# Kernel optimization log

Measured on AMD Instinct MI355X. Metric: run time of the kernel, lower is better.

Reference implementation:

```python
import jax, jax.numpy as jnp
import numpy as np

N = 100000      # nodes
E = 1600000     # edges
F_IN = 128      # num_feat
H = 128         # hidden_dim
EMB = 64        # node_embedding_dim
HL = 256        # hidden_dim_linear


def setup_inputs() -> dict:
    key = jax.random.key(0)
    ks = jax.random.split(key, 12)
    def w(k, fan_in, shape):
        return jax.random.normal(k, shape, dtype=jnp.float32) / np.sqrt(fan_in)
    x = jax.random.normal(ks[0], (N, F_IN), dtype=jnp.float32)
    edge_index = jax.random.randint(ks[1], (2, E), 0, N, dtype=jnp.int32)
    return {
        "x": x,
        "edge_index": edge_index,
        "W0": w(ks[2], F_IN, (F_IN, H)), "b0": jnp.zeros((H,), jnp.float32),
        "W1": w(ks[3], H, (H, H)),       "b1": jnp.zeros((H,), jnp.float32),
        "W2": w(ks[4], H, (H, EMB)),     "b2": jnp.zeros((EMB,), jnp.float32),
        "lw1": w(ks[5], 2 * EMB, (2 * EMB, HL)), "lb1": jnp.zeros((HL,), jnp.float32),
        "lw2": w(ks[6], HL, (HL, 1)),            "lb2": jnp.zeros((1,), jnp.float32),
    }


def _gcn_forward(x, edge_index, W0, b0, W1, b1, W2, b2, lw1, lb1, lw2, lb2):
    src, dst = edge_index[0], edge_index[1]
    # add self loops (PyG GCNConv default) -- shared across layers
    loop = jnp.arange(N, dtype=src.dtype)
    s = jnp.concatenate([src, loop])
    d = jnp.concatenate([dst, loop])
    # symmetric normalization: deg counts incoming edges incl. self loop (>=1)
    deg = jax.ops.segment_sum(jnp.ones_like(d, dtype=x.dtype), d, num_segments=N)
    norm = jax.lax.rsqrt(deg[s] * deg[d])  # [E+N]

    def conv(h, W, b):
        hw = h @ W                                   # small GEMM [N, out]
        msg = hw[s] * norm[:, None]                  # gather + scale [E+N, out]
        agg = jax.ops.segment_sum(msg, d, num_segments=N)
        return agg + b

    z = jax.nn.relu(conv(x, W0, b0))
    z = jax.nn.relu(conv(z, W1, b1))
    z = jax.nn.relu(conv(z, W2, b2))                 # [N, EMB]  (dropout: eval mode, no-op)

    # edge classifier: gather both endpoints, cat, MLP, sigmoid
    h = jnp.concatenate([z[src], z[dst]], axis=1)    # [E, 2*EMB]
    h = jax.nn.relu(h @ lw1 + lb1)
    return jax.nn.sigmoid(h @ lw2 + lb2)             # [E, 1]


def reference(x, edge_index, W0, b0, W1, b1, W2, b2, lw1, lb1, lw2, lb2):
    return _gcn_forward(x, edge_index, W0, b0, W1, b1, W2, b2, lw1, lb1, lw2, lb2)
```

## Files before the change

### kernel.cpp

```cpp
#include <hip/hip_runtime.h>

#define NNODES 100000
#define NEDGES 1600000
#define NBLK 391
#define NSLICE 8
#define SLICEW 12500

typedef __attribute__((ext_vector_type(8))) short bf16x8;
typedef __attribute__((ext_vector_type(4))) float f32x4;

__device__ __forceinline__ unsigned short f2bf(float f) {
  unsigned int u = __float_as_uint(f);
  u = (u + 0x7FFFu + ((u >> 16) & 1u)) >> 16;
  return (unsigned short)u;
}
__device__ __forceinline__ float bf2f(unsigned short h) {
  return __uint_as_float(((unsigned int)h) << 16);
}

__global__ void count_kernel(const int* __restrict__ dst, int* __restrict__ cntD) {
  int slice = blockIdx.x & (NSLICE - 1);
  int e = (blockIdx.x >> 3) * 256 + threadIdx.x;
  if (e >= NEDGES) return;
  int d = dst[e];
  int lo = slice * SLICEW;
  if (d >= lo && d < lo + SLICEW) atomicAdd(&cntD[d], 1);
}

__global__ void scanA_kernel(const int* __restrict__ cntD, int* __restrict__ blockSum) {
  __shared__ int sh[256];
  int v = blockIdx.x * 256 + threadIdx.x;
  sh[threadIdx.x] = (v < NNODES) ? cntD[v] : 0;
  __syncthreads();
  for (int off = 128; off; off >>= 1) {
    if (threadIdx.x < off) sh[threadIdx.x] += sh[threadIdx.x + off];
    __syncthreads();
  }
  if (threadIdx.x == 0) blockSum[blockIdx.x] = sh[0];
}

__global__ void scanB_kernel(int* __restrict__ blockSum) {
  int lane = threadIdx.x;
  int carry = 0;
  for (int base = 0; base < NBLK; base += 64) {
    int i = base + lane;
    int c = (i < NBLK) ? blockSum[i] : 0;
    int pre = c;
#pragma unroll
    for (int off = 1; off < 64; off <<= 1) {
      int t = __shfl_up(pre, off);
      if (lane >= off) pre += t;
    }
    int tot = __shfl(pre, 63);
    if (i < NBLK) blockSum[i] = carry + pre - c;
    carry += tot;
  }
}

__global__ void scanC_kernel(const int* __restrict__ cntD, const int* __restrict__ blockSum,
                             int* __restrict__ startD, int* __restrict__ curD,
                             float* __restrict__ dis) {
  __shared__ int sh[256];
  int tid = threadIdx.x;
  int v = blockIdx.x * 256 + tid;
  int c = (v < NNODES) ? cntD[v] : 0;
  sh[tid] = c;
  __syncthreads();
  for (int off = 1; off < 256; off <<= 1) {
    int t = (tid >= off) ? sh[tid - off] : 0;
    __syncthreads();
    sh[tid] += t;
    __syncthreads();
  }
  if (v < NNODES) {
    int s = blockSum[blockIdx.x] + sh[tid] - c;
    startD[v] = s;
    curD[v] = s;
    dis[v] = rsqrtf((float)(c + 1));
  }
}

__global__ void fill_kernel(const int* __restrict__ src, const int* __restrict__ dst,
                            int* __restrict__ curD, int2* __restrict__ csrPair) {
  int slice = blockIdx.x & (NSLICE - 1);
  int e = (blockIdx.x >> 3) * 256 + threadIdx.x;
  if (e >= NEDGES) return;
  int d = dst[e];
  int lo = slice * SLICEW;
  if (d < lo || d >= lo + SLICEW) return;
  int s = src[e];
  int pd = atomicAdd(&curD[d], 1);
  csrPair[pd] = make_int2(s, e);
}

template <int K, int HOUT>
__global__ void pack_w_kernel(const float* __restrict__ W, unsigned short* __restrict__ Wp) {
  int idx = blockIdx.x * 256 + threadIdx.x;
  if (idx < K * HOUT) {
    int k = idx / HOUT, c = idx - k * HOUT;
    Wp[((size_t)((k >> 5) * HOUT + c)) * 32 + (k & 31)] = f2bf(W[idx]);
  }
}

__global__ void pack_lw1_kernel(const float* __restrict__ lw1, const float* __restrict__ lb1,
                                unsigned short* __restrict__ Wp, float* __restrict__ biasAB) {
  int idx = blockIdx.x * 256 + threadIdx.x;
  if (idx < 64 * 512) {
    int k = idx / 512, c = idx - k * 512;
    float v = (c < 256) ? lw1[k * 256 + c] : lw1[(64 + k) * 256 + (c - 256)];
    Wp[((size_t)((k >> 5) * 512 + c)) * 32 + (k & 31)] = f2bf(v);
  }
  if (idx < 512) biasAB[idx] = (idx < 256) ? lb1[idx] : 0.0f;
}

__global__ void cvt_x_kernel(const float* __restrict__ x, unsigned short* __restrict__ hi,
                             unsigned short* __restrict__ lo) {
  int idx = blockIdx.x * 256 + threadIdx.x;
  if (idx < NNODES * 32) {
    float4 v = ((const float4*)x)[idx];
    ushort4 h, l;
    h.x = f2bf(v.x); l.x = f2bf(v.x - bf2f(h.x));
    h.y = f2bf(v.y); l.y = f2bf(v.y - bf2f(h.y));
    h.z = f2bf(v.z); l.z = f2bf(v.z - bf2f(h.z));
    h.w = f2bf(v.w); l.w = f2bf(v.w - bf2f(h.w));
    ((ushort4*)hi)[idx] = h;
    ((ushort4*)lo)[idx] = l;
  }
}

template <int K, int HOUT, bool SCALE, bool BIAS>
__global__ __launch_bounds__(256)
void mgemm_kernel(const unsigned short* __restrict__ Xhi, const unsigned short* __restrict__ Xlo,
                  const unsigned short* __restrict__ Wp, const float* __restrict__ dis,
                  const float* __restrict__ bias, unsigned short* __restrict__ outb) {
  constexpr int KC = K / 32;
  const int tid = threadIdx.x;
  const int wave = tid >> 6;
  const int lane = tid & 63;
  const int lrow = lane & 15;
  const int lsub = lane >> 4;
  const int rowBase = blockIdx.x * 64 + wave * 16;
  int arow = rowBase + lrow;
  if (arow > NNODES - 1) arow = NNODES - 1;
  bf16x8 ahi[KC], alo[KC];
#pragma unroll
  for (int kc = 0; kc < KC; ++kc) {
    ahi[kc] = *(const bf16x8*)&Xhi[(size_t)arow * K + kc * 32 + lsub * 8];
    alo[kc] = *(const bf16x8*)&Xlo[(size_t)arow * K + kc * 32 + lsub * 8];
  }
  int orow[4];
  float dis4[4];
#pragma unroll
  for (int i = 0; i < 4; ++i) {
    orow[i] = rowBase + lsub * 4 + i;
    int rc = orow[i] < NNODES ? orow[i] : NNODES - 1;
    dis4[i] = SCALE ? dis[rc] : 1.0f;
  }
  for (int ct = 0; ct < HOUT / 16; ++ct) {
    int c = ct * 16 + lrow;
    f32x4 acc = {0.f, 0.f, 0.f, 0.f};
#pragma unroll
    for (int kc = 0; kc < KC; ++kc) {
      bf16x8 b = *(const bf16x8*)&Wp[((size_t)(kc * HOUT + c)) * 32 + lsub * 8];
      acc = __builtin_amdgcn_mfma_f32_16x16x32_bf16(ahi[kc], b, acc, 0, 0, 0);
      acc = __builtin_amdgcn_mfma_f32_16x16x32_bf16(alo[kc], b, acc, 0, 0, 0);
    }
    float bb = BIAS ? bias[c] : 0.0f;
#pragma unroll
    for (int i = 0; i < 4; ++i) {
      if (orow[i] < NNODES) {
        float v = acc[i];
        if (SCALE) v *= dis4[i];
        if (BIAS) v += bb;
        outb[(size_t)orow[i] * HOUT + c] = f2bf(v);
      }
    }
  }
}

template <int HOUT>
__global__ __launch_bounds__(256)
void agg_kernel(const unsigned short* __restrict__ hws, const int2* __restrict__ csrPair,
                const int* __restrict__ startA, const int* __restrict__ cnt,
                const float* __restrict__ dis, const float* __restrict__ bias,
                unsigned short* __restrict__ outHi, unsigned short* __restrict__ outLo) {
  int gid = blockIdx.x * 256 + threadIdx.x;
  int v = gid >> 6;
  int lane = gid & 63;
  constexpr int PER = HOUT / 64;
  float acc0 = 0.0f, acc1 = 0.0f;
  if constexpr (PER == 2) {
    unsigned int o = *(const unsigned int*)&hws[(size_t)v * HOUT + lane * 2];
    acc0 = __uint_as_float(o << 16);
    acc1 = __uint_as_float(o & 0xffff0000u);
  } else {
    acc0 = bf2f(hws[(size_t)v * HOUT + lane]);
  }
  int s0 = startA[v], c = cnt[v];
  for (int base = 0; base < c; base += 64) {
    int rem = c - base;
    int m = rem < 64 ? rem : 64;
    int idx = 0;
    if (lane < m) idx = csrPair[s0 + base + lane].x;
    int j = 0;
    for (; j + 4 <= m; j += 4) {
      int u0 = __shfl(idx, j);
      int u1 = __shfl(idx, j + 1);
      int u2 = __shfl(idx, j + 2);
      int u3 = __shfl(idx, j + 3);
      if constexpr (PER == 2) {
        unsigned int r0 = *(const unsigned int*)&hws[(size_t)u0 * HOUT + lane * 2];
        unsigned int r1 = *(const unsigned int*)&hws[(size_t)u1 * HOUT + lane * 2];
        unsigned int r2 = *(const unsigned int*)&hws[(size_t)u2 * HOUT + lane * 2];
        unsigned int r3 = *(const unsigned int*)&hws[(size_t)u3 * HOUT + lane * 2];
        acc0 += __uint_as_float(r0 << 16) + __uint_as_float(r1 << 16) +
                __uint_as_float(r2 << 16) + __uint_as_float(r3 << 16);
        acc1 += __uint_as_float(r0 & 0xffff0000u) + __uint_as_float(r1 & 0xffff0000u) +
                __uint_as_float(r2 & 0xffff0000u) + __uint_as_float(r3 & 0xffff0000u);
      } else {
        float r0 = bf2f(hws[(size_t)u0 * HOUT + lane]);
        float r1 = bf2f(hws[(size_t)u1 * HOUT + lane]);
        float r2 = bf2f(hws[(size_t)u2 * HOUT + lane]);
        float r3 = bf2f(hws[(size_t)u3 * HOUT + lane]);
        acc0 += (r0 + r1) + (r2 + r3);
      }
    }
    for (; j < m; ++j) {
      int u = __shfl(idx, j);
      if constexpr (PER == 2) {
        unsigned int r = *(const unsigned int*)&hws[(size_t)u * HOUT + lane * 2];
        acc0 += __uint_as_float(r << 16);
        acc1 += __uint_as_float(r & 0xffff0000u);
      } else {
        acc0 += bf2f(hws[(size_t)u * HOUT + lane]);
      }
    }
  }
  float d = dis[v];
  if constexpr (PER == 2) {
    float o0 = fmaf(d, acc0, bias[lane * 2]);
    float o1 = fmaf(d, acc1, bias[lane * 2 + 1]);
    o0 = o0 > 0.0f ? o0 : 0.0f;
    o1 = o1 > 0.0f ? o1 : 0.0f;
    ushort2 h, l;
    h.x = f2bf(o0); l.x = f2bf(o0 - bf2f(h.x));
    h.y = f2bf(o1); l.y = f2bf(o1 - bf2f(h.y));
    *(ushort2*)&outHi[(size_t)v * HOUT + lane * 2] = h;
    *(ushort2*)&outLo[(size_t)v * HOUT + lane * 2] = l;
  } else {
    float o0 = fmaf(d, acc0, bias[lane]);
    o0 = o0 > 0.0f ? o0 : 0.0f;
    unsigned short h = f2bf(o0);
    outHi[(size_t)v * HOUT + lane] = h;
    outLo[(size_t)v * HOUT + lane] = f2bf(o0 - bf2f(h));
  }
}

__global__ __launch_bounds__(256)
void edge_kernel(const unsigned short* __restrict__ AB,
                 const int2* __restrict__ csrPair,
                 const int* __restrict__ startD, const int* __restrict__ cntD,
                 const float* __restrict__ lw2,
                 float* __restrict__ out) {
  int gid = blockIdx.x * 256 + threadIdx.x;
  int v = gid >> 6;
  int lane = gid & 63;
  int sub = lane & 15;
  const unsigned int* Brow = (const unsigned int*)&AB[(size_t)v * 512 + 256 + sub * 16];
  uint4 br0 = *(const uint4*)Brow;
  uint4 br1 = *(const uint4*)(Brow + 4);
  float bq[16];
  {
    unsigned int u[8] = {br0.x, br0.y, br0.z, br0.w, br1.x, br1.y, br1.z, br1.w};
#pragma unroll
    for (int i = 0; i < 8; ++i) {
      bq[2 * i]     = __uint_as_float(u[i] << 16);
      bq[2 * i + 1] = __uint_as_float(u[i] & 0xffff0000u);
    }
  }
  float wv[16];
#pragma unroll
  for (int i = 0; i < 4; ++i) {
    float4 w4 = *(const float4*)&lw2[sub * 16 + i * 4];
    wv[4 * i] = w4.x; wv[4 * i + 1] = w4.y; wv[4 * i + 2] = w4.z; wv[4 * i + 3] = w4.w;
  }

  int s0 = startD[v], c = cntD[v];
  for (int base = 0; base < c; base += 64) {
    int rem = c - base;
    int m = rem < 64 ? rem : 64;
    int sj = 0, ej = 0;
    if (lane < m) {
      int2 p = csrPair[s0 + base + lane];
      sj = p.x; ej = p.y;
    }
    for (int j = 0; j < m; j += 4) {
      int ls = j + (lane >> 4);
      int lsc = ls < m ? ls : m - 1;
      int s = __shfl(sj, lsc);
      int e = __shfl(ej, lsc);
      const unsigned int* Arow = (const unsigned int*)&AB[(size_t)(unsigned)s * 512 + sub * 16];
      uint4 a0 = *(const uint4*)Arow;
      uint4 a1 = *(const uint4*)(Arow + 4);
      unsigned int au[8] = {a0.x, a0.y, a0.z, a0.w, a1.x, a1.y, a1.z, a1.w};
      float p0 = 0.f, p1 = 0.f, p2 = 0.f, p3 = 0.f;
#pragma unroll
      for (int i = 0; i < 4; ++i) {
        float hlo0 = __uint_as_float(au[2 * i] << 16) + bq[4 * i];
        float hhi0 = __uint_as_float(au[2 * i] & 0xffff0000u) + bq[4 * i + 1];
        float hlo1 = __uint_as_float(au[2 * i + 1] << 16) + bq[4 * i + 2];
        float hhi1 = __uint_as_float(au[2 * i + 1] & 0xffff0000u) + bq[4 * i + 3];
        hlo0 = hlo0 > 0.f ? hlo0 : 0.f;
        hhi0 = hhi0 > 0.f ? hhi0 : 0.f;
        hlo1 = hlo1 > 0.f ? hlo1 : 0.f;
        hhi1 = hhi1 > 0.f ? hhi1 : 0.f;
        p0 = fmaf(hlo0, wv[4 * i], p0);
        p1 = fmaf(hhi0, wv[4 * i + 1], p1);
        p2 = fmaf(hlo1, wv[4 * i + 2], p2);
        p3 = fmaf(hhi1, wv[4 * i + 3], p3);
      }
      float acc = (p0 + p1) + (p2 + p3);
      acc += __shfl_xor(acc, 1);
      acc += __shfl_xor(acc, 2);
      acc += __shfl_xor(acc, 4);
      acc += __shfl_xor(acc, 8);
      if (ls < m && sub == 0) out[e] = acc;
    }
  }
}

__global__ __launch_bounds__(256)
void sigmoid_kernel(float* __restrict__ out, const float* __restrict__ lb2) {
  int i = blockIdx.x * 256 + threadIdx.x;
  if (i < NEDGES) {
    float lb = lb2[0];
    out[i] = 1.0f / (1.0f + expf(-(out[i] + lb)));
  }
}

extern "C" void kernel_launch(void* const* d_in, const int* in_sizes, int n_in,
                              void* d_out, int out_size, void* d_ws, size_t ws_size,
                              hipStream_t stream) {
  const float* x   = (const float*)d_in[0];
  const int*   ei  = (const int*)d_in[1];
  const float* W0  = (const float*)d_in[2];
  const float* b0  = (const float*)d_in[3];
  const float* W1  = (const float*)d_in[4];
  const float* b1  = (const float*)d_in[5];
  const float* W2  = (const float*)d_in[6];
  const float* b2  = (const float*)d_in[7];
  const float* lw1 = (const float*)d_in[8];
  const float* lb1 = (const float*)d_in[9];
  const float* lw2 = (const float*)d_in[10];
  const float* lb2 = (const float*)d_in[11];
  float* out = (float*)d_out;
  const int* src = ei;
  const int* dst = ei + NEDGES;

  char* ws = (char*)d_ws;
  size_t off = 0;
  auto alloc = [&](size_t bytes) -> void* {
    void* p = ws + off;
    off += (bytes + 255) & ~(size_t)255;
    return p;
  };
  int*   cntD   = (int*)alloc((size_t)NNODES * 4);
  int*   startD = (int*)alloc((size_t)NNODES * 4);
  int*   curD   = (int*)alloc((size_t)NNODES * 4);
  float* dis    = (float*)alloc((size_t)NNODES * 4);
  int*   blockSum = (int*)alloc((size_t)NBLK * 4);
  int2*  csrPair= (int2*)alloc((size_t)NEDGES * 8);
  unsigned short* P16  = (unsigned short*)alloc((size_t)NNODES * 128 * 2);
  unsigned short* XQhi = (unsigned short*)alloc((size_t)NNODES * 128 * 2);
  unsigned short* XQlo = (unsigned short*)alloc((size_t)NNODES * 128 * 2);
  unsigned short* AB   = (unsigned short*)alloc((size_t)NNODES * 512 * 2);
  unsigned short* Wp0  = (unsigned short*)alloc((size_t)128 * 128 * 2);
  unsigned short* Wp1  = (unsigned short*)alloc((size_t)128 * 128 * 2);
  unsigned short* Wp2  = (unsigned short*)alloc((size_t)128 * 64 * 2);
  unsigned short* WpE  = (unsigned short*)alloc((size_t)64 * 512 * 2);
  float* biasAB = (float*)alloc(512 * 4);

  const int EB8 = NSLICE * ((NEDGES + 255) / 256);

  hipMemsetAsync(cntD, 0, (size_t)NNODES * 4, stream);
  count_kernel<<<EB8, 256, 0, stream>>>(dst, cntD);
  scanA_kernel<<<NBLK, 256, 0, stream>>>(cntD, blockSum);
  scanB_kernel<<<1, 64, 0, stream>>>(blockSum);
  scanC_kernel<<<NBLK, 256, 0, stream>>>(cntD, blockSum, startD, curD, dis);
  fill_kernel<<<EB8, 256, 0, stream>>>(src, dst, curD, csrPair);

  pack_w_kernel<128, 128><<<64, 256, 0, stream>>>(W0, Wp0);
  pack_w_kernel<128, 128><<<64, 256, 0, stream>>>(W1, Wp1);
  pack_w_kernel<128, 64><<<32, 256, 0, stream>>>(W2, Wp2);
  pack_lw1_kernel<<<128, 256, 0, stream>>>(lw1, lb1, WpE, biasAB);
  cvt_x_kernel<<<(NNODES * 32 + 255) / 256, 256, 0, stream>>>(x, XQhi, XQlo);

  const int GB = (NNODES + 63) / 64;
  const int AB_ = (NNODES * 64) / 256;

  mgemm_kernel<128, 128, true, false><<<GB, 256, 0, stream>>>(XQhi, XQlo, Wp0, dis, nullptr, P16);
  agg_kernel<128><<<AB_, 256, 0, stream>>>(P16, csrPair, startD, cntD, dis, b0, XQhi, XQlo);
  mgemm_kernel<128, 128, true, false><<<GB, 256, 0, stream>>>(XQhi, XQlo, Wp1, dis, nullptr, P16);
  agg_kernel<128><<<AB_, 256, 0, stream>>>(P16, csrPair, startD, cntD, dis, b1, XQhi, XQlo);
  mgemm_kernel<128, 64, true, false><<<GB, 256, 0, stream>>>(XQhi, XQlo, Wp2, dis, nullptr, P16);
  agg_kernel<64><<<AB_, 256, 0, stream>>>(P16, csrPair, startD, cntD, dis, b2, XQhi, XQlo);

  mgemm_kernel<64, 512, false, true><<<GB, 256, 0, stream>>>(XQhi, XQlo, WpE, nullptr, biasAB, AB);

  edge_kernel<<<AB_, 256, 0, stream>>>(AB, csrPair, startD, cntD, lw2, out);
  sigmoid_kernel<<<(NEDGES + 255) / 256, 256, 0, stream>>>(out, lb2);
}
```

Before: 615.7 us.

## Fuse x conversion into first GEMM, sigmoid into edge kernel, use packed fp16 edge math

Drops the separate x hi/lo conversion kernel by converting fp32 x to bf16 hi/lo inside the first GEMM's operand load. Folds the sigmoid and bias into the edge classifier kernel so the output is written once rather than written and re-read. Stores the edge-MLP projection in fp16 and evaluates add/relu/dot with packed fp16 instructions (v_pk_add_f16, v_pk_max_f16, v_dot2_f32_f16), handling two edges per lane-group iteration for more memory-level parallelism. Doing the hidden activations in fp16 lowers precision and risks overflow or rounding differences compared with the fp32 path.

```diff
diff --git a/kernel.cpp b/kernel.cpp
--- a/kernel.cpp
+++ b/kernel.cpp
@@ -16,6 +16,22 @@
 }
 __device__ __forceinline__ float bf2f(unsigned short h) {
   return __uint_as_float(((unsigned int)h) << 16);
+}
+
+__device__ __forceinline__ unsigned int pk_add_f16(unsigned int a, unsigned int b) {
+  unsigned int r;
+  asm("v_pk_add_f16 %0, %1, %2" : "=v"(r) : "v"(a), "v"(b));
+  return r;
+}
+__device__ __forceinline__ unsigned int pk_max0_f16(unsigned int a, unsigned int z) {
+  unsigned int r;
+  asm("v_pk_max_f16 %0, %1, %2" : "=v"(r) : "v"(a), "v"(z));
+  return r;
+}
+__device__ __forceinline__ float dot2_f16(unsigned int a, unsigned int b, float c) {
+  float r;
+  asm("v_dot2_f32_f16 %0, %1, %2, %3" : "=v"(r) : "v"(a), "v"(b), "v"(c));
+  return r;
 }
 
 __global__ void count_kernel(const int* __restrict__ dst, int* __restrict__ cntD) {
@@ -103,7 +119,9 @@
 }
 
 __global__ void pack_lw1_kernel(const float* __restrict__ lw1, const float* __restrict__ lb1,
-                                unsigned short* __restrict__ Wp, float* __restrict__ biasAB) {
+                                const float* __restrict__ lw2,
+                                unsigned short* __restrict__ Wp, float* __restrict__ biasAB,
+                                unsigned int* __restrict__ wh) {
   int idx = blockIdx.x * 256 + threadIdx.x;
   if (idx < 64 * 512) {
     int k = idx / 512, c = idx - k * 512;
@@ -111,28 +129,20 @@
     Wp[((size_t)((k >> 5) * 512 + c)) * 32 + (k & 31)] = f2bf(v);
   }
   if (idx < 512) biasAB[idx] = (idx < 256) ? lb1[idx] : 0.0f;
-}
-
-__global__ void cvt_x_kernel(const float* __restrict__ x, unsigned short* __restrict__ hi,
-                             unsigned short* __restrict__ lo) {
-  int idx = blockIdx.x * 256 + threadIdx.x;
-  if (idx < NNODES * 32) {
-    float4 v = ((const float4*)x)[idx];
-    ushort4 h, l;
-    h.x = f2bf(v.x); l.x = f2bf(v.x - bf2f(h.x));
-    h.y = f2bf(v.y); l.y = f2bf(v.y - bf2f(h.y));
-    h.z = f2bf(v.z); l.z = f2bf(v.z - bf2f(h.z));
-    h.w = f2bf(v.w); l.w = f2bf(v.w - bf2f(h.w));
-    ((ushort4*)hi)[idx] = h;
-    ((ushort4*)lo)[idx] = l;
-  }
-}
-
-template <int K, int HOUT, bool SCALE, bool BIAS>
+  if (idx < 128) {
+    _Float16 lo = (_Float16)lw2[idx * 2];
+    _Float16 hi = (_Float16)lw2[idx * 2 + 1];
+    unsigned short ulo = __builtin_bit_cast(unsigned short, lo);
+    unsigned short uhi = __builtin_bit_cast(unsigned short, hi);
+    wh[idx] = (unsigned int)ulo | ((unsigned int)uhi << 16);
+  }
+}
+
+template <int K, int HOUT, bool SCALE, bool BIAS, bool F32IN, bool F16OUT>
 __global__ __launch_bounds__(256)
-void mgemm_kernel(const unsigned short* __restrict__ Xhi, const unsigned short* __restrict__ Xlo,
+void mgemm_kernel(const void* __restrict__ Xhi_v, const void* __restrict__ Xlo_v,
                   const unsigned short* __restrict__ Wp, const float* __restrict__ dis,
-                  const float* __restrict__ bias, unsigned short* __restrict__ outb) {
+                  const float* __restrict__ bias, void* __restrict__ outv) {
   constexpr int KC = K / 32;
   const int tid = threadIdx.x;
   const int wave = tid >> 6;
@@ -143,10 +153,28 @@
   int arow = rowBase + lrow;
   if (arow > NNODES - 1) arow = NNODES - 1;
   bf16x8 ahi[KC], alo[KC];
-#pragma unroll
-  for (int kc = 0; kc < KC; ++kc) {
-    ahi[kc] = *(const bf16x8*)&Xhi[(size_t)arow * K + kc * 32 + lsub * 8];
-    alo[kc] = *(const bf16x8*)&Xlo[(size_t)arow * K + kc * 32 + lsub * 8];
+  if constexpr (F32IN) {
+    const float* xf = (const float*)Xhi_v;
+#pragma unroll
+    for (int kc = 0; kc < KC; ++kc) {
+      float4 v0 = *(const float4*)&xf[(size_t)arow * K + kc * 32 + lsub * 8];
+      float4 v1 = *(const float4*)&xf[(size_t)arow * K + kc * 32 + lsub * 8 + 4];
+      float fv[8] = {v0.x, v0.y, v0.z, v0.w, v1.x, v1.y, v1.z, v1.w};
+#pragma unroll
+      for (int i = 0; i < 8; ++i) {
+        unsigned short h = f2bf(fv[i]);
+        ahi[kc][i] = (short)h;
+        alo[kc][i] = (short)f2bf(fv[i] - bf2f(h));
+      }
+    }
+  } else {
+    const unsigned short* Xhi = (const unsigned short*)Xhi_v;
+    const unsigned short* Xlo = (const unsigned short*)Xlo_v;
+#pragma unroll
+    for (int kc = 0; kc < KC; ++kc) {
+      ahi[kc] = *(const bf16x8*)&Xhi[(size_t)arow * K + kc * 32 + lsub * 8];
+      alo[kc] = *(const bf16x8*)&Xlo[(size_t)arow * K + kc * 32 + lsub * 8];
+    }
   }
   int orow[4];
   float dis4[4];
@@ -172,7 +200,11 @@
         float v = acc[i];
         if (SCALE) v *= dis4[i];
         if (BIAS) v += bb;
-        outb[(size_t)orow[i] * HOUT + c] = f2bf(v);
+        if constexpr (F16OUT) {
+          ((_Float16*)outv)[(size_t)orow[i] * HOUT + c] = (_Float16)v;
+        } else {
+          ((unsigned short*)outv)[(size_t)orow[i] * HOUT + c] = f2bf(v);
+        }
       }
     }
   }
@@ -257,33 +289,30 @@
 }
 
 __global__ __launch_bounds__(256)
-void edge_kernel(const unsigned short* __restrict__ AB,
+void edge_kernel(const unsigned int* __restrict__ AB32,
                  const int2* __restrict__ csrPair,
                  const int* __restrict__ startD, const int* __restrict__ cntD,
-                 const float* __restrict__ lw2,
+                 const unsigned int* __restrict__ wh, const float* __restrict__ lb2,
                  float* __restrict__ out) {
   int gid = blockIdx.x * 256 + threadIdx.x;
   int v = gid >> 6;
   int lane = gid & 63;
   int sub = lane & 15;
-  const unsigned int* Brow = (const unsigned int*)&AB[(size_t)v * 512 + 256 + sub * 16];
-  uint4 br0 = *(const uint4*)Brow;
-  uint4 br1 = *(const uint4*)(Brow + 4);
-  float bq[16];
+  unsigned int zero = 0u;
+  unsigned int bu[8], wu[8];
   {
-    unsigned int u[8] = {br0.x, br0.y, br0.z, br0.w, br1.x, br1.y, br1.z, br1.w};
-#pragma unroll
-    for (int i = 0; i < 8; ++i) {
-      bq[2 * i]     = __uint_as_float(u[i] << 16);
-      bq[2 * i + 1] = __uint_as_float(u[i] & 0xffff0000u);
-    }
-  }
-  float wv[16];
-#pragma unroll
-  for (int i = 0; i < 4; ++i) {
-    float4 w4 = *(const float4*)&lw2[sub * 16 + i * 4];
-    wv[4 * i] = w4.x; wv[4 * i + 1] = w4.y; wv[4 * i + 2] = w4.z; wv[4 * i + 3] = w4.w;
-  }
+    const unsigned int* Brow = AB32 + (size_t)v * 256 + 128 + sub * 8;
+    uint4 b0 = *(const uint4*)Brow;
+    uint4 b1 = *(const uint4*)(Brow + 4);
+    bu[0] = b0.x; bu[1] = b0.y; bu[2] = b0.z; bu[3] = b0.w;
+    bu[4] = b1.x; bu[5] = b1.y; bu[6] = b1.z; bu[7] = b1.w;
+    const unsigned int* W = wh + sub * 8;
+    uint4 w0 = *(const uint4*)W;
+    uint4 w1 = *(const uint4*)(W + 4);
+    wu[0] = w0.x; wu[1] = w0.y; wu[2] = w0.z; wu[3] = w0.w;
+    wu[4] = w1.x; wu[5] = w1.y; wu[6] = w1.z; wu[7] = w1.w;
+  }
+  float lb = lb2[0];
 
   int s0 = startD[v], c = cntD[v];
   for (int base = 0; base < c; base += 64) {
@@ -294,47 +323,42 @@
       int2 p = csrPair[s0 + base + lane];
       sj = p.x; ej = p.y;
     }
-    for (int j = 0; j < m; j += 4) {
-      int ls = j + (lane >> 4);
-      int lsc = ls < m ? ls : m - 1;
-      int s = __shfl(sj, lsc);
-      int e = __shfl(ej, lsc);
-      const unsigned int* Arow = (const unsigned int*)&AB[(size_t)(unsigned)s * 512 + sub * 16];
-      uint4 a0 = *(const uint4*)Arow;
-      uint4 a1 = *(const uint4*)(Arow + 4);
-      unsigned int au[8] = {a0.x, a0.y, a0.z, a0.w, a1.x, a1.y, a1.z, a1.w};
-      float p0 = 0.f, p1 = 0.f, p2 = 0.f, p3 = 0.f;
-#pragma unroll
-      for (int i = 0; i < 4; ++i) {
-        float hlo0 = __uint_as_float(au[2 * i] << 16) + bq[4 * i];
-        float hhi0 = __uint_as_float(au[2 * i] & 0xffff0000u) + bq[4 * i + 1];
-        float hlo1 = __uint_as_float(au[2 * i + 1] << 16) + bq[4 * i + 2];
-        float hhi1 = __uint_as_float(au[2 * i + 1] & 0xffff0000u) + bq[4 * i + 3];
-        hlo0 = hlo0 > 0.f ? hlo0 : 0.f;
-        hhi0 = hhi0 > 0.f ? hhi0 : 0.f;
-        hlo1 = hlo1 > 0.f ? hlo1 : 0.f;
-        hhi1 = hhi1 > 0.f ? hhi1 : 0.f;
-        p0 = fmaf(hlo0, wv[4 * i], p0);
-        p1 = fmaf(hhi0, wv[4 * i + 1], p1);
-        p2 = fmaf(hlo1, wv[4 * i + 2], p2);
-        p3 = fmaf(hhi1, wv[4 * i + 3], p3);
+    int g = lane >> 4;
+    for (int j = 0; j < m; j += 8) {
+      int ls0 = j + g, ls1 = j + 4 + g;
+      int l0 = ls0 < m ? ls0 : m - 1;
+      int l1 = ls1 < m ? ls1 : m - 1;
+      int sA = __shfl(sj, l0);
+      int eA = __shfl(ej, l0);
+      int sB = __shfl(sj, l1);
+      int eB = __shfl(ej, l1);
+      const unsigned int* ArowA = AB32 + (size_t)(unsigned)sA * 256 + sub * 8;
+      const unsigned int* ArowB = AB32 + (size_t)(unsigned)sB * 256 + sub * 8;
+      uint4 a00 = *(const uint4*)ArowA;
+      uint4 a01 = *(const uint4*)(ArowA + 4);
+      uint4 a10 = *(const uint4*)ArowB;
+      uint4 a11 = *(const uint4*)(ArowB + 4);
+      unsigned int au0[8] = {a00.x, a00.y, a00.z, a00.w, a01.x, a01.y, a01.z, a01.w};
+      unsigned int au1[8] = {a10.x, a10.y, a10.z, a10.w, a11.x, a11.y, a11.z, a11.w};
+      float acc0 = 0.f, acc1 = 0.f;
+#pragma unroll
+      for (int i = 0; i < 8; ++i) {
+        unsigned int h0 = pk_max0_f16(pk_add_f16(au0[i], bu[i]), zero);
+        acc0 = dot2_f16(h0, wu[i], acc0);
+        unsigned int h1 = pk_max0_f16(pk_add_f16(au1[i], bu[i]), zero);
+        acc1 = dot2_f16(h1, wu[i], acc1);
       }
-      float acc = (p0 + p1) + (p2 + p3);
-      acc += __shfl_xor(acc, 1);
-      acc += __shfl_xor(acc, 2);
-      acc += __shfl_xor(acc, 4);
-      acc += __shfl_xor(acc, 8);
-      if (ls < m && sub == 0) out[e] = acc;
-    }
-  }
-}
-
-__global__ __launch_bounds__(256)
-void sigmoid_kernel(float* __restrict__ out, const float* __restrict__ lb2) {
-  int i = blockIdx.x * 256 + threadIdx.x;
-  if (i < NEDGES) {
-    float lb = lb2[0];
-    out[i] = 1.0f / (1.0f + expf(-(out[i] + lb)));
+      acc0 += __shfl_xor(acc0, 1);
+      acc0 += __shfl_xor(acc0, 2);
+      acc0 += __shfl_xor(acc0, 4);
+      acc0 += __shfl_xor(acc0, 8);
+      acc1 += __shfl_xor(acc1, 1);
+      acc1 += __shfl_xor(acc1, 2);
+      acc1 += __shfl_xor(acc1, 4);
+      acc1 += __shfl_xor(acc1, 8);
+      if (ls0 < m && sub == 0) out[eA] = 1.0f / (1.0f + expf(-(acc0 + lb)));
+      if (ls1 < m && sub == 0) out[eB] = 1.0f / (1.0f + expf(-(acc1 + lb)));
+    }
   }
 }
 
@@ -373,12 +397,13 @@
   unsigned short* P16  = (unsigned short*)alloc((size_t)NNODES * 128 * 2);
   unsigned short* XQhi = (unsigned short*)alloc((size_t)NNODES * 128 * 2);
   unsigned short* XQlo = (unsigned short*)alloc((size_t)NNODES * 128 * 2);
-  unsigned short* AB   = (unsigned short*)alloc((size_t)NNODES * 512 * 2);
+  void*           AB   = alloc((size_t)NNODES * 512 * 2);
   unsigned short* Wp0  = (unsigned short*)alloc((size_t)128 * 128 * 2);
   unsigned short* Wp1  = (unsigned short*)alloc((size_t)128 * 128 * 2);
   unsigned short* Wp2  = (unsigned short*)alloc((size_t)128 * 64 * 2);
   unsigned short* WpE  = (unsigned short*)alloc((size_t)64 * 512 * 2);
   float* biasAB = (float*)alloc(512 * 4);
+  unsigned int* wh = (unsigned int*)alloc(128 * 4);
 
   const int EB8 = NSLICE * ((NEDGES + 255) / 256);
 
@@ -392,21 +417,19 @@
   pack_w_kernel<128, 128><<<64, 256, 0, stream>>>(W0, Wp0);
   pack_w_kernel<128, 128><<<64, 256, 0, stream>>>(W1, Wp1);
   pack_w_kernel<128, 64><<<32, 256, 0, stream>>>(W2, Wp2);
-  pack_lw1_kernel<<<128, 256, 0, stream>>>(lw1, lb1, WpE, biasAB);
-  cvt_x_kernel<<<(NNODES * 32 + 255) / 256, 256, 0, stream>>>(x, XQhi, XQlo);
+  pack_lw1_kernel<<<128, 256, 0, stream>>>(lw1, lb1, lw2, WpE, biasAB, wh);
 
   const int GB = (NNODES + 63) / 64;
   const int AB_ = (NNODES * 64) / 256;
 
-  mgemm_kernel<128, 128, true, false><<<GB, 256, 0, stream>>>(XQhi, XQlo, Wp0, dis, nullptr, P16);
+  mgemm_kernel<128, 128, true, false, true, false><<<GB, 256, 0, stream>>>(x, nullptr, Wp0, dis, nullptr, P16);
   agg_kernel<128><<<AB_, 256, 0, stream>>>(P16, csrPair, startD, cntD, dis, b0, XQhi, XQlo);
-  mgemm_kernel<128, 128, true, false><<<GB, 256, 0, stream>>>(XQhi, XQlo, Wp1, dis, nullptr, P16);
+  mgemm_kernel<128, 128, true, false, false, false><<<GB, 256, 0, stream>>>(XQhi, XQlo, Wp1, dis, nullptr, P16);
   agg_kernel<128><<<AB_, 256, 0, stream>>>(P16, csrPair, startD, cntD, dis, b1, XQhi, XQlo);
-  mgemm_kernel<128, 64, true, false><<<GB, 256, 0, stream>>>(XQhi, XQlo, Wp2, dis, nullptr, P16);
+  mgemm_kernel<128, 64, true, false, false, false><<<GB, 256, 0, stream>>>(XQhi, XQlo, Wp2, dis, nullptr, P16);
   agg_kernel<64><<<AB_, 256, 0, stream>>>(P16, csrPair, startD, cntD, dis, b2, XQhi, XQlo);
 
-  mgemm_kernel<64, 512, false, true><<<GB, 256, 0, stream>>>(XQhi, XQlo, WpE, nullptr, biasAB, AB);
-
-  edge_kernel<<<AB_, 256, 0, stream>>>(AB, csrPair, startD, cntD, lw2, out);
-  sigmoid_kernel<<<(NEDGES + 255) / 256, 256, 0, stream>>>(out, lb2);
-}
+  mgemm_kernel<64, 512, false, true, false, true><<<GB, 256, 0, stream>>>(XQhi, XQlo, WpE, nullptr, biasAB, AB);
+
+  edge_kernel<<<AB_, 256, 0, stream>>>((const unsigned int*)AB, csrPair, startD, cntD, wh, lb2, out);
+}
```

After: 594.8 us. 3.4% less time.
